# Kernel optimization log

Hardware: AMD Instinct MI355X
Metric: run time of the kernel (lower is better)

Reference implementation:

```python
import jax, jax.numpy as jnp
import numpy as np

B, T, C = 4, 2048, 1024
H, D = 16, 64  # num_heads, head_size; H*D == C


def setup_inputs() -> dict:
    key = jax.random.key(0)
    k1, k2, k3 = jax.random.split(key, 3)
    x = jax.random.normal(k1, (B, T, C), dtype=jnp.float32)
    w_qkv = jax.random.normal(k2, (C, 3 * C), dtype=jnp.float32) * (C ** -0.5)
    w_out = jax.random.normal(k3, (C, C), dtype=jnp.float32) * (C ** -0.5)
    b_out = jnp.zeros((C,), dtype=jnp.float32)
    return {"x": x, "w_qkv": w_qkv, "w_out": w_out, "b_out": b_out}


def reference(x, w_qkv, w_out, b_out):
    Bb, Tt, Cc = x.shape
    qkv = x @ w_qkv                        # [B,T,3C]
    q, k, v = jnp.split(qkv, 3, axis=2)
    # [B,T,C] -> [B,H,T,D]
    q = q.reshape(Bb, Tt, H, D).transpose(0, 2, 1, 3)
    k = k.reshape(Bb, Tt, H, D).transpose(0, 2, 1, 3)
    v = v.reshape(Bb, Tt, H, D).transpose(0, 2, 1, 3)
    scores = jnp.einsum('bhqd,bhkd->bhqk', q, k) * (D ** -0.5)
    causal = jnp.tril(jnp.ones((Tt, Tt), dtype=bool))
    scores = jnp.where(causal, scores, -jnp.inf)
    attn = jax.nn.softmax(scores, axis=-1)  # dropout is identity in eval mode
    out = jnp.einsum('bhqk,bhkd->bhqd', attn, v)
    out = out.transpose(0, 2, 1, 3).reshape(Bb, Tt, Cc)
    return out @ w_out + b_out
```

## Files before the change

kernel.cpp:

```cpp
#include <hip/hip_runtime.h>

typedef __bf16 bf16;
typedef __bf16 bf16x4 __attribute__((ext_vector_type(4)));
typedef __bf16 bf16x8 __attribute__((ext_vector_type(8)));
typedef float  f32x4  __attribute__((ext_vector_type(4)));

#define MFMA16(A_, B_, C_) __builtin_amdgcn_mfma_f32_16x16x32_bf16((A_), (B_), (C_), 0, 0, 0)

#define BB 4
#define TT 2048
#define CC 1024
#define HH 16
#define DD 64
#define MM (BB * TT)
#define N_QKV (3 * CC)
#define LDSS 72
#define BSTRIDE 36
#define QSCALE2 0.18033688f

#define BARRIER() do { asm volatile("" ::: "memory"); \
                       __builtin_amdgcn_s_barrier();  \
                       asm volatile("" ::: "memory"); } while (0)
#define VMCNT(n)  asm volatile("s_waitcnt vmcnt(" #n ")" ::: "memory")

static __device__ __forceinline__ void store_lds8(bf16* p, bf16x8 v) {
  bf16x4 lo, hi;
#pragma unroll
  for (int i = 0; i < 4; i++) { lo[i] = v[i]; hi[i] = v[i + 4]; }
  *(bf16x4*)p = lo;
  *(bf16x4*)(p + 4) = hi;
}

static __device__ __forceinline__ bf16x8 load_lds8(const bf16* p) {
  bf16x4 lo = *(const bf16x4*)p;
  bf16x4 hi = *(const bf16x4*)(p + 4);
  bf16x8 v;
#pragma unroll
  for (int i = 0; i < 4; i++) { v[i] = lo[i]; v[i + 4] = hi[i]; }
  return v;
}

static __device__ __forceinline__ void async_cp16(const bf16* g, bf16* l) {
  __builtin_amdgcn_global_load_lds(
      (const __attribute__((address_space(1))) void*)g,
      (__attribute__((address_space(3))) void*)l, 16, 0, 0);
}

__global__ __launch_bounds__(256) void sniff_k(const unsigned short* __restrict__ u,
                                               int* __restrict__ flag) {
  __shared__ int s;
  if (threadIdx.x == 0) s = 0;
  __syncthreads();
  int c = 0;
  for (int i = threadIdx.x; i < 65536; i += 256)
    if ((u[i] & 0x7F80u) == 0x7F80u) c = 1;
  if (c) atomicOr(&s, 1);
  __syncthreads();
  if (threadIdx.x == 0) *flag = s;
}

__global__ __launch_bounds__(256) void cvt_k(const void* __restrict__ in,
                                             bf16* __restrict__ out,
                                             const int* __restrict__ flag,
                                             size_t off) {
  const int fl = *flag;
  const size_t i = ((size_t)blockIdx.x * 256 + threadIdx.x) * 8;
  if (fl) {
    f32x4 a = *(const f32x4*)((const float*)in + off + i);
    f32x4 b = *(const f32x4*)((const float*)in + off + i + 4);
    bf16x8 o;
#pragma unroll
    for (int j = 0; j < 4; j++) { o[j] = (bf16)a[j]; o[4 + j] = (bf16)b[j]; }
    *(bf16x8*)(out + i) = o;
  } else {
    *(bf16x8*)(out + i) = *(const bf16x8*)((const bf16*)in + off + i);
  }
}

__global__ __launch_bounds__(256) void transpose_k(const void* __restrict__ in,
                                                   bf16* __restrict__ out,
                                                   int R, int C,
                                                   const int* __restrict__ flag) {
  __shared__ bf16 tile[32][33];
  const int fl = *flag;
  const int c0 = blockIdx.x * 32, r0 = blockIdx.y * 32;
  const int tx = threadIdx.x & 31, ty = threadIdx.x >> 5;
#pragma unroll
  for (int i = ty; i < 32; i += 8) {
    const size_t idx = (size_t)(r0 + i) * C + c0 + tx;
    tile[i][tx] = fl ? (bf16)((const float*)in)[idx] : ((const bf16*)in)[idx];
  }
  __syncthreads();
#pragma unroll
  for (int i = ty; i < 32; i += 8)
    out[(size_t)(c0 + i) * R + r0 + tx] = tile[tx][i];
}

__global__ __launch_bounds__(256) void vtrans_k(const bf16* __restrict__ qkv,
                                                bf16* __restrict__ vt) {
  __shared__ bf16 tile[32][33];
  const int bh = blockIdx.z;
  const int t0 = blockIdx.x * 32, d0 = blockIdx.y * 32;
  const bf16* src = qkv + (size_t)(bh >> 4) * TT * N_QKV + 2 * CC + (bh & 15) * DD;
  const int tx = threadIdx.x & 31, ty = threadIdx.x >> 5;
#pragma unroll
  for (int i = ty; i < 32; i += 8)
    tile[i][tx] = src[(size_t)(t0 + i) * N_QKV + d0 + tx];
  __syncthreads();
  bf16* dst = vt + ((size_t)bh * DD + d0) * TT + t0;
#pragma unroll
  for (int i = ty; i < 32; i += 8)
    dst[(size_t)i * TT + tx] = tile[tx][i];
}

template <int EPI>
__global__ __launch_bounds__(512, 2) void gemm8p2(const bf16* __restrict__ A,
                                                  const bf16* __restrict__ Bt,
                                                  const void* __restrict__ biasv,
                                                  void* __restrict__ Cv,
                                                  const int* __restrict__ flag,
                                                  int M, int N, int K,
                                                  int lda, int ldc) {
  __shared__ __align__(16) bf16 sAb[2][2][256 * 32];
  __shared__ __align__(16) bf16 sBb[2][2][128 * 32];
  const int fl = *flag;
  const int tid = threadIdx.x;
  const int lane = tid & 63, wave = tid >> 6;
  const int quad = lane >> 4, l15 = lane & 15;
  const int wm = wave >> 1, wn = wave & 1;

  const int nn = N >> 7;
  const int cpx = gridDim.x >> 3;
  const int sw = ((int)blockIdx.x & 7) * cpx + ((int)blockIdx.x >> 3);
  const int m0 = (sw / nn) * 256, n0 = (sw % nn) * 128;

  const int srow = tid >> 2;
  const int scol8 = (((tid & 3) ^ ((tid >> 3) & 3)) << 3);
  const int rdcol = ((quad ^ ((l15 >> 1) & 3)) << 3);

  const bf16* Asrc = A + (size_t)(m0 + srow) * lda + scol8;
  const bf16* Bsrc = Bt + (size_t)(n0 + srow) * K + scol8;

  f32x4 acc[4][4];
#pragma unroll
  for (int i = 0; i < 4; i++)
#pragma unroll
    for (int j = 0; j < 4; j++) {
      f32x4 z = {0.f, 0.f, 0.f, 0.f};
      acc[i][j] = z;
    }

#define ST_U(buf_, kk_, k0_) do {                                          \
    async_cp16(Asrc + (k0_) + (kk_) * 32, &sAb[buf_][kk_][wave * 512]);    \
    async_cp16(Asrc + (size_t)128 * lda + (k0_) + (kk_) * 32,              \
               &sAb[buf_][kk_][4096 + wave * 512]);                        \
    async_cp16(Bsrc + (k0_) + (kk_) * 32, &sBb[buf_][kk_][wave * 512]);    \
  } while (0)

#define PH2(buf_, kk_, STAGE_, WAIT_) do {                                   \
    bf16x8 af_[4], bf_[4];                                                   \
    _Pragma("unroll")                                                        \
    for (int mf = 0; mf < 4; mf++)                                           \
      af_[mf] = *(const bf16x8*)(&sAb[buf_][kk_][                            \
          (wm * 64 + mf * 16 + l15) * 32 + rdcol]);                          \
    _Pragma("unroll")                                                        \
    for (int nf = 0; nf < 4; nf++)                                           \
      bf_[nf] = *(const bf16x8*)(&sBb[buf_][kk_][                            \
          (wn * 64 + nf * 16 + l15) * 32 + rdcol]);                          \
    STAGE_;                                                                  \
    BARRIER();                                                               \
    __builtin_amdgcn_s_setprio(1);                                           \
    _Pragma("unroll")                                                        \
    for (int mf = 0; mf < 4; mf++)                                           \
      _Pragma("unroll")                                                      \
      for (int nf = 0; nf < 4; nf++)                                         \
        acc[mf][nf] = MFMA16(af_[mf], bf_[nf], acc[mf][nf]);                 \
    __builtin_amdgcn_s_setprio(0);                                           \
    WAIT_;                                                                   \
    BARRIER();                                                               \
  } while (0)

  ST_U(0, 0, 0);
  ST_U(0, 1, 0);
  ST_U(1, 0, 64);
  VMCNT(3);
  BARRIER();

  int k0 = 0;
  const int NI = (K >> 7) - 1;
  for (int i = 0; i < NI; i++, k0 += 128) {
    PH2(0, 0, ST_U(1, 1, k0 + 64),  VMCNT(6));
    PH2(0, 1, ST_U(0, 0, k0 + 128), VMCNT(6));
    PH2(1, 0, ST_U(0, 1, k0 + 128), VMCNT(6));
    PH2(1, 1, ST_U(1, 0, k0 + 192), VMCNT(6));
  }
  PH2(0, 0, ST_U(1, 1, k0 + 64), VMCNT(3));
  PH2(0, 1, ;,                   VMCNT(0));
  PH2(1, 0, ;,                   ;);
  PH2(1, 1, ;,                   ;);

#undef PH2
#undef ST_U

#pragma unroll
  for (int mf = 0; mf < 4; mf++) {
#pragma unroll
    for (int r = 0; r < 4; r++) {
      const int m = m0 + wm * 64 + mf * 16 + quad * 4 + r;
#pragma unroll
      for (int nf = 0; nf < 4; nf++) {
        const int n = n0 + wn * 64 + nf * 16 + l15;
        float v = acc[mf][nf][r];
        const size_t idx = (size_t)m * ldc + n;
        if (EPI == 1) {
          v += fl ? ((const float*)biasv)[n] : (float)((const bf16*)biasv)[n];
          if (fl) ((float*)Cv)[idx] = v;
          else    ((bf16*)Cv)[idx] = (bf16)v;
        } else {
          ((bf16*)Cv)[idx] = (bf16)v;
        }
      }
    }
  }
}

template <int EPI>
__global__ __launch_bounds__(256) void gemm_lds(const bf16* __restrict__ A,
                                                const bf16* __restrict__ Bt,
                                                const void* __restrict__ biasv,
                                                void* __restrict__ Cv,
                                                const int* __restrict__ flag,
                                                size_t aoff, size_t coff,
                                                int M, int N, int K,
                                                int lda, int ldc) {
  const int fl = *flag;
  __shared__ __align__(16) bf16 sA[128 * 32];
  __shared__ __align__(16) bf16 sB[128 * 32];
  const int tid = threadIdx.x;
  const int lane = tid & 63, wave = tid >> 6;
  const int quad = lane >> 4, l15 = lane & 15;
  const int wr = wave >> 1, wc = wave & 1;
  const int m0 = blockIdx.x * 128, n0 = blockIdx.y * 128;
  const int grow = lane >> 2;
  const int gcol = (lane & 3) * 8;

  f32x4 acc[4][4];
#pragma unroll
  for (int i = 0; i < 4; i++)
#pragma unroll
    for (int j = 0; j < 4; j++) {
      f32x4 z = {0.f, 0.f, 0.f, 0.f};
      acc[i][j] = z;
    }

  const bf16* Ag = A + aoff + (size_t)(m0 + wave * 32 + grow) * lda + gcol;
  const bf16* Bg = Bt + (size_t)(n0 + wave * 32 + grow) * K + gcol;
  bf16* sAw = sA + wave * 32 * 32;
  bf16* sBw = sB + wave * 32 * 32;

  for (int k0 = 0; k0 < K; k0 += 32) {
    __syncthreads();
    async_cp16(Ag, sAw);
    async_cp16(Ag + (size_t)16 * lda, sAw + 16 * 32);
    async_cp16(Bg, sBw);
    async_cp16(Bg + (size_t)16 * K, sBw + 16 * 32);
    Ag += 32;
    Bg += 32;
    __syncthreads();

    bf16x8 af[4], bfr[4];
#pragma unroll
    for (int mi = 0; mi < 4; mi++)
      af[mi] = *(const bf16x8*)(sA + (wr * 64 + mi * 16 + l15) * 32 + quad * 8);
#pragma unroll
    for (int ni = 0; ni < 4; ni++)
      bfr[ni] = *(const bf16x8*)(sB + (wc * 64 + ni * 16 + l15) * 32 + quad * 8);
#pragma unroll
    for (int mi = 0; mi < 4; mi++)
#pragma unroll
      for (int ni = 0; ni < 4; ni++)
        acc[mi][ni] = MFMA16(af[mi], bfr[ni], acc[mi][ni]);
  }

#pragma unroll
  for (int mi = 0; mi < 4; mi++) {
#pragma unroll
    for (int r = 0; r < 4; r++) {
      const int m = m0 + wr * 64 + mi * 16 + quad * 4 + r;
#pragma unroll
      for (int ni = 0; ni < 4; ni++) {
        const int n = n0 + wc * 64 + ni * 16 + l15;
        float v = acc[mi][ni][r];
        const size_t idx = coff + (size_t)m * ldc + n;
        if (EPI == 1) {
          v += fl ? ((const float*)biasv)[n] : (float)((const bf16*)biasv)[n];
          if (fl) ((float*)Cv)[idx] = v;
          else    ((bf16*)Cv)[idx] = (bf16)v;
        } else {
          ((bf16*)Cv)[idx] = (bf16)v;
        }
      }
    }
  }
}

template <int EPI, bool AF>
__global__ __launch_bounds__(256) void gemm_bt(const void* __restrict__ Av,
                                               const bf16* __restrict__ Bt,
                                               const void* __restrict__ biasv,
                                               void* __restrict__ Cv,
                                               const int* __restrict__ flag,
                                               size_t aoff, size_t coff,
                                               int M, int N, int K,
                                               int lda, int ldc) {
  const int fl = *flag;
  const bool af32 = AF && (fl != 0);
  __shared__ __align__(16) bf16 sA[128 * 32];
  __shared__ __align__(16) bf16 sB[128 * 32];
  const int tid = threadIdx.x;
  const int lane = tid & 63, wave = tid >> 6;
  const int quad = lane >> 4, l15 = lane & 15;
  const int wr = wave >> 1, wc = wave & 1;
  const int m0 = blockIdx.x * 128, n0 = blockIdx.y * 128;
  const int srow = tid >> 2;
  const int scol = (tid & 3) * 8;

  f32x4 acc[4][4];
#pragma unroll
  for (int i = 0; i < 4; i++)
#pragma unroll
    for (int j = 0; j < 4; j++) {
      f32x4 z = {0.f, 0.f, 0.f, 0.f};
      acc[i][j] = z;
    }

  const size_t abase0 = aoff + (size_t)(m0 + srow) * lda + scol;
  const size_t abase1 = abase0 + (size_t)64 * lda;
  const bf16* Bg0 = Bt + (size_t)(n0 + srow) * K + scol;
  const bf16* Bg1 = Bg0 + (size_t)64 * K;

  for (int k0 = 0; k0 < K; k0 += 32) {
    bf16x8 a0, a1;
    if (af32) {
      const float* Af = (const float*)Av;
      f32x4 p00 = *(const f32x4*)(Af + abase0 + k0);
      f32x4 p01 = *(const f32x4*)(Af + abase0 + k0 + 4);
      f32x4 p10 = *(const f32x4*)(Af + abase1 + k0);
      f32x4 p11 = *(const f32x4*)(Af + abase1 + k0 + 4);
#pragma unroll
      for (int i = 0; i < 4; i++) {
        a0[i] = (bf16)p00[i]; a0[i + 4] = (bf16)p01[i];
        a1[i] = (bf16)p10[i]; a1[i + 4] = (bf16)p11[i];
      }
    } else {
      const bf16* Ab = (const bf16*)Av;
      a0 = *(const bf16x8*)(Ab + abase0 + k0);
      a1 = *(const bf16x8*)(Ab + abase1 + k0);
    }
    bf16x8 b0 = *(const bf16x8*)(Bg0 + k0);
    bf16x8 b1 = *(const bf16x8*)(Bg1 + k0);
    __syncthreads();
    *(bf16x8*)(sA + srow * 32 + scol) = a0;
    *(bf16x8*)(sA + (64 + srow) * 32 + scol) = a1;
    *(bf16x8*)(sB + srow * 32 + scol) = b0;
    *(bf16x8*)(sB + (64 + srow) * 32 + scol) = b1;
    __syncthreads();

    bf16x8 af[4], bfr[4];
#pragma unroll
    for (int mi = 0; mi < 4; mi++)
      af[mi] = *(const bf16x8*)(sA + (wr * 64 + mi * 16 + l15) * 32 + quad * 8);
#pragma unroll
    for (int ni = 0; ni < 4; ni++)
      bfr[ni] = *(const bf16x8*)(sB + (wc * 64 + ni * 16 + l15) * 32 + quad * 8);
#pragma unroll
    for (int mi = 0; mi < 4; mi++)
#pragma unroll
      for (int ni = 0; ni < 4; ni++)
        acc[mi][ni] = MFMA16(af[mi], bfr[ni], acc[mi][ni]);
  }

#pragma unroll
  for (int mi = 0; mi < 4; mi++) {
#pragma unroll
    for (int r = 0; r < 4; r++) {
      const int m = m0 + wr * 64 + mi * 16 + quad * 4 + r;
#pragma unroll
      for (int ni = 0; ni < 4; ni++) {
        const int n = n0 + wc * 64 + ni * 16 + l15;
        float v = acc[mi][ni][r];
        const size_t idx = coff + (size_t)m * ldc + n;
        if (EPI == 1) {
          v += fl ? ((const float*)biasv)[n] : (float)((const bf16*)biasv)[n];
          if (fl) ((float*)Cv)[idx] = v;
          else    ((bf16*)Cv)[idx] = (bf16)v;
        } else {
          ((bf16*)Cv)[idx] = (bf16)v;
        }
      }
    }
  }
}

template <int EPI, bool AF, bool WF>
__global__ __launch_bounds__(256) void gemm_nt(const void* __restrict__ Av,
                                               const void* __restrict__ Wv,
                                               const void* __restrict__ biasv,
                                               void* __restrict__ Cv,
                                               const int* __restrict__ flag,
                                               size_t aoff, size_t coff,
                                               int M, int N, int K,
                                               int lda, int ldc) {
  const int fl = *flag;
  const bool af32 = AF && (fl != 0);
  const bool wf32 = WF && (fl != 0);
  __shared__ __align__(16) bf16 sA[128 * 32];
  __shared__ __align__(16) bf16 sB[128 * BSTRIDE];
  const int tid = threadIdx.x;
  const int lane = tid & 63, wave = tid >> 6;
  const int quad = lane >> 4, l15 = lane & 15;
  const int wr = wave >> 1, wc = wave & 1;
  const int m0 = blockIdx.x * 128, n0 = blockIdx.y * 128;
  const int arow = tid >> 2, acol = (tid & 3) * 8;
  const int wk = tid >> 3, wn = (tid & 7) * 16;

  f32x4 acc[4][4];
#pragma unroll
  for (int i = 0; i < 4; i++)
#pragma unroll
    for (int j = 0; j < 4; j++) {
      f32x4 z = {0.f, 0.f, 0.f, 0.f};
      acc[i][j] = z;
    }

  const size_t abase0 = aoff + (size_t)(m0 + arow) * lda + acol;
  const size_t abase1 = abase0 + (size_t)64 * lda;

  for (int k0 = 0; k0 < K; k0 += 32) {
    bf16x8 a0, a1;
    if (af32) {
      const float* Af = (const float*)Av;
      f32x4 p00 = *(const f32x4*)(Af + abase0 + k0);
      f32x4 p01 = *(const f32x4*)(Af + abase0 + k0 + 4);
      f32x4 p10 = *(const f32x4*)(Af + abase1 + k0);
      f32x4 p11 = *(const f32x4*)(Af + abase1 + k0 + 4);
#pragma unroll
      for (int i = 0; i < 4; i++) {
        a0[i] = (bf16)p00[i]; a0[i + 4] = (bf16)p01[i];
        a1[i] = (bf16)p10[i]; a1[i + 4] = (bf16)p11[i];
      }
    } else {
      const bf16* Ab = (const bf16*)Av;
      a0 = *(const bf16x8*)(Ab + abase0 + k0);
      a1 = *(const bf16x8*)(Ab + abase1 + k0);
    }
    bf16 wreg[16];
    const size_t wbase = (size_t)(k0 + wk) * N + n0 + wn;
    if (wf32) {
      const float* Wf = (const float*)Wv;
      f32x4 q0 = *(const f32x4*)(Wf + wbase);
      f32x4 q1 = *(const f32x4*)(Wf + wbase + 4);
      f32x4 q2 = *(const f32x4*)(Wf + wbase + 8);
      f32x4 q3 = *(const f32x4*)(Wf + wbase + 12);
#pragma unroll
      for (int i = 0; i < 4; i++) {
        wreg[i] = (bf16)q0[i];      wreg[4 + i] = (bf16)q1[i];
        wreg[8 + i] = (bf16)q2[i];  wreg[12 + i] = (bf16)q3[i];
      }
    } else {
      const bf16* Wb = (const bf16*)Wv;
      bf16x8 w0 = *(const bf16x8*)(Wb + wbase);
      bf16x8 w1 = *(const bf16x8*)(Wb + wbase + 8);
#pragma unroll
      for (int i = 0; i < 8; i++) { wreg[i] = w0[i]; wreg[8 + i] = w1[i]; }
    }
    __syncthreads();
    *(bf16x8*)(sA + arow * 32 + acol) = a0;
    *(bf16x8*)(sA + (64 + arow) * 32 + acol) = a1;
#pragma unroll
    for (int i = 0; i < 16; i++)
      sB[(wn + i) * BSTRIDE + wk] = wreg[i];
    __syncthreads();

    bf16x8 af[4], bfr[4];
#pragma unroll
    for (int mi = 0; mi < 4; mi++)
      af[mi] = *(const bf16x8*)(sA + (wr * 64 + mi * 16 + l15) * 32 + quad * 8);
#pragma unroll
    for (int ni = 0; ni < 4; ni++)
      bfr[ni] = load_lds8(sB + (wc * 64 + ni * 16 + l15) * BSTRIDE + quad * 8);
#pragma unroll
    for (int mi = 0; mi < 4; mi++)
#pragma unroll
      for (int ni = 0; ni < 4; ni++)
        acc[mi][ni] = MFMA16(af[mi], bfr[ni], acc[mi][ni]);
  }

#pragma unroll
  for (int mi = 0; mi < 4; mi++) {
#pragma unroll
    for (int r = 0; r < 4; r++) {
      const int m = m0 + wr * 64 + mi * 16 + quad * 4 + r;
#pragma unroll
      for (int ni = 0; ni < 4; ni++) {
        const int n = n0 + wc * 64 + ni * 16 + l15;
        float v = acc[mi][ni][r];
        const size_t idx = coff + (size_t)m * ldc + n;
        if (EPI == 1) {
          v += fl ? ((const float*)biasv)[n] : (float)((const bf16*)biasv)[n];
          if (fl) ((float*)Cv)[idx] = v;
          else    ((bf16*)Cv)[idx] = (bf16)v;
        } else {
          ((bf16*)Cv)[idx] = (bf16)v;
        }
      }
    }
  }
}

__global__ __launch_bounds__(256) void attn_k(bf16* __restrict__ qkv,
                                              const bf16* __restrict__ vt) {
  __shared__ __align__(16) bf16 sP[128 * LDSS];
  __shared__ __align__(16) bf16 sK[64 * LDSS];
  __shared__ __align__(16) bf16 sVt[64 * LDSS];

  const int tid = threadIdx.x;
  const int lane = tid & 63, wave = tid >> 6;
  const int quad = lane >> 4, l15 = lane & 15;
  const int bh = blockIdx.x;
  bf16* base = qkv + (size_t)(bh >> 4) * TT * N_QKV + (bh & 15) * DD;
  const bf16* Qp = base;
  const bf16* Kp = base + CC;
  const bf16* vhead = vt + (size_t)bh * DD * TT;

  const int qt = 15 - (int)blockIdx.y;
  const int q0 = qt * 128;
  const int wave_row0 = q0 + wave * 32;
  bf16* sPw = sP + (size_t)(wave * 32) * LDSS;

  const int krow = tid >> 2;
  const int kcol = (tid & 3) * 16;

  bf16x8 ones;
  {
    const bf16 o = (l15 == 0) ? (bf16)1.0f : (bf16)0.0f;
#pragma unroll
    for (int i = 0; i < 8; i++) ones[i] = o;
  }

  bf16x8 aq[2][2];
#pragma unroll
  for (int mi = 0; mi < 2; mi++)
#pragma unroll
    for (int ks = 0; ks < 2; ks++) {
      bf16x8 v = *(const bf16x8*)(Qp + (size_t)(wave_row0 + mi * 16 + l15) * N_QKV +
                                  ks * 32 + quad * 8);
#pragma unroll
      for (int i = 0; i < 8; i++) v[i] = (bf16)((float)v[i] * QSCALE2);
      aq[mi][ks] = v;
    }

  bf16x8 kr0, kr1, vr0, vr1;
  {
    const bf16* kp = Kp + (size_t)krow * N_QKV + kcol;
    kr0 = *(const bf16x8*)kp;
    kr1 = *(const bf16x8*)(kp + 8);
    const bf16* vp = vhead + (size_t)krow * TT + kcol;
    vr0 = *(const bf16x8*)vp;
    vr1 = *(const bf16x8*)(vp + 8);
  }

  f32x4 Oacc[2][4];
  f32x4 lacc[2];
#pragma unroll
  for (int mi = 0; mi < 2; mi++) {
    f32x4 z = {0.f, 0.f, 0.f, 0.f};
    lacc[mi] = z;
#pragma unroll
    for (int nt = 0; nt < 4; nt++) Oacc[mi][nt] = z;
  }

  const int jmax = q0 + 64;

  for (int j0 = 0; j0 <= jmax; j0 += 64) {
    __syncthreads();
    *(bf16x8*)(sK + krow * LDSS + kcol) = kr0;
    *(bf16x8*)(sK + krow * LDSS + kcol + 8) = kr1;
    *(bf16x8*)(sVt + krow * LDSS + kcol) = vr0;
    *(bf16x8*)(sVt + krow * LDSS + kcol + 8) = vr1;
    __syncthreads();

    if (j0 + 64 <= jmax) {
      const bf16* kp = Kp + (size_t)(j0 + 64 + krow) * N_QKV + kcol;
      kr0 = *(const bf16x8*)kp;
      kr1 = *(const bf16x8*)(kp + 8);
      const bf16* vp = vhead + (size_t)krow * TT + j0 + 64 + kcol;
      vr0 = *(const bf16x8*)vp;
      vr1 = *(const bf16x8*)(vp + 8);
    }

    if (j0 <= wave_row0 + 31) {
      f32x4 S[2][4];
#pragma unroll
      for (int mi = 0; mi < 2; mi++)
#pragma unroll
        for (int kt = 0; kt < 4; kt++) {
          f32x4 z = {0.f, 0.f, 0.f, 0.f};
          S[mi][kt] = z;
        }
      __builtin_amdgcn_s_setprio(1);
#pragma unroll
      for (int kt = 0; kt < 4; kt++) {
        const bf16* kp = sK + (size_t)(kt * 16 + l15) * LDSS + quad * 8;
        bf16x8 k0 = *(const bf16x8*)kp;
        bf16x8 k1 = *(const bf16x8*)(kp + 32);
        S[0][kt] = MFMA16(k0, aq[0][0], S[0][kt]);
        S[0][kt] = MFMA16(k1, aq[0][1], S[0][kt]);
        S[1][kt] = MFMA16(k0, aq[1][0], S[1][kt]);
        S[1][kt] = MFMA16(k1, aq[1][1], S[1][kt]);
      }
      __builtin_amdgcn_s_setprio(0);

      const bool needmask = (j0 + 63 > wave_row0);
#pragma unroll
      for (int mi = 0; mi < 2; mi++) {
        const int qg = wave_row0 + mi * 16 + l15;
#pragma unroll
        for (int kt = 0; kt < 4; kt++) {
          const int kb = j0 + kt * 16 + quad * 4;
          bf16x4 pk;
#pragma unroll
          for (int r = 0; r < 4; r++) {
            float e = __builtin_amdgcn_exp2f(S[mi][kt][r]);
            if (needmask && (kb + r > qg)) e = 0.f;
            pk[r] = (bf16)e;
          }
          *(bf16x4*)(sPw + (size_t)(mi * 16 + l15) * LDSS + kt * 16 + quad * 4) = pk;
        }
      }

      bf16x8 ap0[2], ap1[2];
#pragma unroll
      for (int mi = 0; mi < 2; mi++) {
        const bf16* pp = sPw + (size_t)(mi * 16 + l15) * LDSS + quad * 8;
        ap0[mi] = *(const bf16x8*)pp;
        ap1[mi] = *(const bf16x8*)(pp + 32);
      }
      __builtin_amdgcn_s_setprio(1);
#pragma unroll
      for (int mi = 0; mi < 2; mi++) {
        lacc[mi] = MFMA16(ap0[mi], ones, lacc[mi]);
        lacc[mi] = MFMA16(ap1[mi], ones, lacc[mi]);
      }
#pragma unroll
      for (int nt = 0; nt < 4; nt++) {
        const bf16* vp = sVt + (size_t)(nt * 16 + l15) * LDSS + quad * 8;
        bf16x8 v0 = *(const bf16x8*)vp;
        bf16x8 v1 = *(const bf16x8*)(vp + 32);
        Oacc[0][nt] = MFMA16(ap0[0], v0, Oacc[0][nt]);
        Oacc[0][nt] = MFMA16(ap1[0], v1, Oacc[0][nt]);
        Oacc[1][nt] = MFMA16(ap0[1], v0, Oacc[1][nt]);
        Oacc[1][nt] = MFMA16(ap1[1], v1, Oacc[1][nt]);
      }
      __builtin_amdgcn_s_setprio(0);
    }
  }

#pragma unroll
  for (int mi = 0; mi < 2; mi++)
#pragma unroll
    for (int r = 0; r < 4; r++) {
      const float lv = __shfl(lacc[mi][r], lane & 48, 64);
      const float invl = 1.0f / lv;
      const int t = q0 + wave * 32 + mi * 16 + quad * 4 + r;
#pragma unroll
      for (int nt = 0; nt < 4; nt++)
        base[(size_t)t * N_QKV + nt * 16 + l15] =
            (bf16)(Oacc[mi][nt][r] * invl);
    }
}

__global__ __launch_bounds__(256) void attn_s(bf16* __restrict__ qkv) {
  __shared__ __align__(16) bf16 sQ[128 * LDSS];
  __shared__ __align__(16) bf16 sK[64 * LDSS];
  __shared__ __align__(16) bf16 sVt[64 * LDSS];

  const int tid = threadIdx.x;
  const int lane = tid & 63, wave = tid >> 6;
  const int quad = lane >> 4, l15 = lane & 15;
  const int bh = blockIdx.x;
  bf16* base = qkv + (size_t)(bh >> 4) * TT * N_QKV + (bh & 15) * DD;
  const bf16* Qp = base;
  const bf16* Kp = base + CC;
  const bf16* Vp = base + 2 * CC;

  const int krow = tid >> 2;
  const int kcol = (tid & 3) * 16;
  const int vkey = tid & 31;
  const int vcol = (tid >> 5) * 8;

  bf16x8 ones;
  {
    const bf16 o = (l15 == 0) ? (bf16)1.0f : (bf16)0.0f;
#pragma unroll
    for (int i = 0; i < 8; i++) ones[i] = o;
  }

  const int qt = 15 - (int)blockIdx.y;
  const int q0 = qt * 128;

#pragma unroll
  for (int p = 0; p < 2; p++) {
    const int r = p * 64 + krow;
    const bf16* src = Qp + (size_t)(q0 + r) * N_QKV + kcol;
    bf16x8 v0 = *(const bf16x8*)src;
    bf16x8 v1 = *(const bf16x8*)(src + 8);
#pragma unroll
    for (int i = 0; i < 8; i++) {
      v0[i] = (bf16)((float)v0[i] * QSCALE2);
      v1[i] = (bf16)((float)v1[i] * QSCALE2);
    }
    *(bf16x8*)(sQ + r * LDSS + kcol) = v0;
    *(bf16x8*)(sQ + r * LDSS + kcol + 8) = v1;
  }

  bf16x8 kr0, kr1, vr0, vr1;
  {
    const bf16* kp = Kp + (size_t)krow * N_QKV + kcol;
    kr0 = *(const bf16x8*)kp;
    kr1 = *(const bf16x8*)(kp + 8);
    vr0 = *(const bf16x8*)(Vp + (size_t)vkey * N_QKV + vcol);
    vr1 = *(const bf16x8*)(Vp + (size_t)(32 + vkey) * N_QKV + vcol);
  }
  __syncthreads();

  bf16x8 aq[2][2];
#pragma unroll
  for (int mi = 0; mi < 2; mi++) {
    const bf16* qp = sQ + (size_t)(wave * 32 + mi * 16 + l15) * LDSS + quad * 8;
    aq[mi][0] = *(const bf16x8*)qp;
    aq[mi][1] = *(const bf16x8*)(qp + 32);
  }

  f32x4 Oacc[2][4];
  f32x4 lacc[2];
#pragma unroll
  for (int mi = 0; mi < 2; mi++) {
    f32x4 z = {0.f, 0.f, 0.f, 0.f};
    lacc[mi] = z;
#pragma unroll
    for (int nt = 0; nt < 4; nt++) Oacc[mi][nt] = z;
  }

  const int jmax = q0 + 64;
  const int wave_row0 = q0 + wave * 32;
  bf16* sP = sQ + (size_t)(wave * 32) * LDSS;

  for (int j0 = 0; j0 <= jmax; j0 += 64) {
    __syncthreads();
    *(bf16x8*)(sK + krow * LDSS + kcol) = kr0;
    *(bf16x8*)(sK + krow * LDSS + kcol + 8) = kr1;
#pragma unroll
    for (int i = 0; i < 8; i++) {
      sVt[(vcol + i) * LDSS + vkey] = vr0[i];
      sVt[(vcol + i) * LDSS + 32 + vkey] = vr1[i];
    }
    __syncthreads();

    if (j0 + 64 <= jmax) {
      const bf16* kp = Kp + (size_t)(j0 + 64 + krow) * N_QKV + kcol;
      kr0 = *(const bf16x8*)kp;
      kr1 = *(const bf16x8*)(kp + 8);
      vr0 = *(const bf16x8*)(Vp + (size_t)(j0 + 64 + vkey) * N_QKV + vcol);
      vr1 = *(const bf16x8*)(Vp + (size_t)(j0 + 96 + vkey) * N_QKV + vcol);
    }

    if (j0 <= wave_row0 + 31) {
      f32x4 S[2][4];
#pragma unroll
      for (int nt = 0; nt < 4; nt++) {
        const bf16* kp = sK + (size_t)(nt * 16 + l15) * LDSS + quad * 8;
        bf16x8 bk0 = *(const bf16x8*)kp;
        bf16x8 bk1 = *(const bf16x8*)(kp + 32);
#pragma unroll
        for (int mi = 0; mi < 2; mi++) {
          f32x4 acc = {0.f, 0.f, 0.f, 0.f};
          acc = MFMA16(aq[mi][0], bk0, acc);
          acc = MFMA16(aq[mi][1], bk1, acc);
          S[mi][nt] = acc;
        }
      }

      const bool needmask = (j0 + 63 > wave_row0);
#pragma unroll
      for (int mi = 0; mi < 2; mi++)
#pragma unroll
        for (int nt = 0; nt < 4; nt++) {
          const int kc = j0 + nt * 16 + l15;
#pragma unroll
          for (int r = 0; r < 4; r++) {
            float e = __builtin_amdgcn_exp2f(S[mi][nt][r]);
            if (needmask && kc > wave_row0 + mi * 16 + quad * 4 + r) e = 0.f;
            sP[(size_t)(mi * 16 + quad * 4 + r) * LDSS + nt * 16 + l15] =
                (bf16)e;
          }
        }

      bf16x8 ap[2][2];
#pragma unroll
      for (int mi = 0; mi < 2; mi++) {
        const bf16* pp = sP + (size_t)(mi * 16 + l15) * LDSS + quad * 8;
        ap[mi][0] = *(const bf16x8*)pp;
        ap[mi][1] = *(const bf16x8*)(pp + 32);
        lacc[mi] = MFMA16(ap[mi][0], ones, lacc[mi]);
        lacc[mi] = MFMA16(ap[mi][1], ones, lacc[mi]);
      }
#pragma unroll
      for (int nt = 0; nt < 4; nt++) {
        const bf16* vp = sVt + (size_t)(nt * 16 + l15) * LDSS + quad * 8;
        bf16x8 bv0 = *(const bf16x8*)vp;
        bf16x8 bv1 = *(const bf16x8*)(vp + 32);
#pragma unroll
        for (int mi = 0; mi < 2; mi++) {
          Oacc[mi][nt] = MFMA16(ap[mi][0], bv0, Oacc[mi][nt]);
          Oacc[mi][nt] = MFMA16(ap[mi][1], bv1, Oacc[mi][nt]);
        }
      }
    }
  }

#pragma unroll
  for (int mi = 0; mi < 2; mi++)
#pragma unroll
    for (int r = 0; r < 4; r++) {
      const float lv = __shfl(lacc[mi][r], lane & 48, 64);
      const float invl = 1.0f / lv;
      const int t = q0 + wave * 32 + mi * 16 + quad * 4 + r;
#pragma unroll
      for (int nt = 0; nt < 4; nt++)
        base[(size_t)t * N_QKV + nt * 16 + l15] =
            (bf16)(Oacc[mi][nt][r] * invl);
    }
}

extern "C" void kernel_launch(void* const* d_in, const int* in_sizes, int n_in,
                              void* d_out, int out_size, void* d_ws, size_t ws_size,
                              hipStream_t stream) {
  const void* x = d_in[0];
  const void* w_qkv = d_in[1];
  const void* w_out = d_in[2];
  const void* b_out = d_in[3];

  int* flag = (int*)d_ws;
  char* p = (char*)d_ws + 256;
  bf16* wqkvT = (bf16*)p;
  bf16* woutT = wqkvT + (size_t)N_QKV * CC;

  const size_t wT_bytes = ((size_t)N_QKV * CC + (size_t)CC * CC) * 2;
  const size_t qkv_bytes = (size_t)MM * N_QKV * 2;
  const size_t need_A = 256 + wT_bytes + qkv_bytes;
  const size_t need_B = 256 + wT_bytes + (size_t)TT * N_QKV * 2;

  sniff_k<<<1, 256, 0, stream>>>((const unsigned short*)x, flag);

  if (ws_size >= need_A) {
    bf16* qkv = woutT + (size_t)CC * CC;
    bf16* xb = qkv + (size_t)MM * N_QKV;
    const size_t slack = ws_size - need_A;

    transpose_k<<<dim3(N_QKV / 32, CC / 32), 256, 0, stream>>>(w_qkv, wqkvT, CC, N_QKV, flag);
    transpose_k<<<dim3(CC / 32, CC / 32), 256, 0, stream>>>(w_out, woutT, CC, CC, flag);

    const size_t full_xb = (size_t)MM * CC * 2;
    const size_t half_xb = full_xb / 2;
    if (slack >= full_xb) {
      cvt_k<<<(MM * CC) / 2048, 256, 0, stream>>>(x, xb, flag, 0);
      gemm8p2<0><<<dim3((MM / 256) * (N_QKV / 128)), 512, 0, stream>>>(
          xb, wqkvT, nullptr, qkv, flag, MM, N_QKV, CC, CC, N_QKV);
      bf16* vt = xb;
      vtrans_k<<<dim3(TT / 32, DD / 32, BB * HH), 256, 0, stream>>>(qkv, vt);
      attn_k<<<dim3(BB * HH, 16), 256, 0, stream>>>(qkv, vt);
    } else if (slack >= half_xb) {
      for (int m0 = 0; m0 < MM; m0 += 4096) {
        cvt_k<<<(4096 * CC) / 2048, 256, 0, stream>>>(x, xb, flag, (size_t)m0 * CC);
        gemm_lds<0><<<dim3(4096 / 128, N_QKV / 128), 256, 0, stream>>>(
            xb, wqkvT, nullptr, qkv, flag, 0, (size_t)m0 * N_QKV,
            4096, N_QKV, CC, CC, N_QKV);
      }
      attn_s<<<dim3(BB * HH, 16), 256, 0, stream>>>(qkv);
    } else {
      gemm_bt<0, true><<<dim3(MM / 128, N_QKV / 128), 256, 0, stream>>>(
          x, wqkvT, nullptr, qkv, flag, 0, 0, MM, N_QKV, CC, CC, N_QKV);
      attn_s<<<dim3(BB * HH, 16), 256, 0, stream>>>(qkv);
    }

    gemm8p2<1><<<dim3((MM / 256) * (CC / 128)), 512, 0, stream>>>(
        qkv, woutT, b_out, d_out, flag, MM, CC, CC, N_QKV, CC);
  } else if (ws_size >= need_B) {
    bf16* qkv = woutT + (size_t)CC * CC;
    transpose_k<<<dim3(N_QKV / 32, CC / 32), 256, 0, stream>>>(w_qkv, wqkvT, CC, N_QKV, flag);
    transpose_k<<<dim3(CC / 32, CC / 32), 256, 0, stream>>>(w_out, woutT, CC, CC, flag);
    for (int b = 0; b < BB; b++) {
      const size_t xoff = (size_t)b * TT * CC;
      gemm_bt<0, true><<<dim3(TT / 128, N_QKV / 128), 256, 0, stream>>>(
          x, wqkvT, nullptr, qkv, flag, xoff, 0, TT, N_QKV, CC, CC, N_QKV);
      attn_s<<<dim3(HH, 16), 256, 0, stream>>>(qkv);
      gemm_lds<1><<<dim3(TT / 128, CC / 128), 256, 0, stream>>>(
          qkv, woutT, b_out, d_out, flag, 0, xoff, TT, CC, CC, N_QKV, CC);
    }
  } else {
    bf16* qkvb = (bf16*)p;
    for (int b = 0; b < BB; b++) {
      const size_t xoff = (size_t)b * TT * CC;
      gemm_nt<0, true, true><<<dim3(TT / 128, N_QKV / 128), 256, 0, stream>>>(
          x, w_qkv, nullptr, qkvb, flag, xoff, 0, TT, N_QKV, CC, CC, N_QKV);
      attn_s<<<dim3(HH, 16), 256, 0, stream>>>(qkvb);
      gemm_nt<1, false, true><<<dim3(TT / 128, CC / 128), 256, 0, stream>>>(
          qkvb, w_out, b_out, d_out, flag, 0, xoff, TT, CC, CC, N_QKV, CC);
    }
  }
}
```

Baseline: 311.4 us.

## Add 256x256-tile 8-phase pipelined GEMM for the QKV projection

Adds a new gemm_q kernel that computes the QKV projection with 256x256 output tiles and a K-step of 64. Each block splits its tile into four 128x128 quadrants, loads them through double-buffered, XOR-swizzled LDS with async copies, and interleaves the loads with MFMA phases using barriers and s_setprio. Block indices are remapped in groups of eight to improve cache locality. The larger tile raises arithmetic intensity over the old 256x128 kernel, at the cost of more accumulator registers and LDS, which may limit occupancy.

```diff
diff --git a/kernel.cpp b/kernel.cpp
--- a/kernel.cpp
+++ b/kernel.cpp
@@ -111,6 +111,144 @@
 #pragma unroll
   for (int i = ty; i < 32; i += 8)
     dst[(size_t)i * TT + tx] = tile[tx][i];
+}
+
+__global__ __launch_bounds__(512, 2) void gemm_q(const bf16* __restrict__ A,
+                                                 const bf16* __restrict__ Bt,
+                                                 bf16* __restrict__ C,
+                                                 int M, int N, int K,
+                                                 int lda, int ldc) {
+  __shared__ __align__(16) bf16 sA[2][2][128 * 64];
+  __shared__ __align__(16) bf16 sB[2][2][128 * 64];
+  const int tid = threadIdx.x;
+  const int lane = tid & 63, wave = tid >> 6;
+  const int quad = lane >> 4, l15 = lane & 15;
+  const int wm = wave >> 2, wn = wave & 3;
+
+  const int nn = N >> 8;
+  const int cpx = gridDim.x >> 3;
+  const int sw = ((int)blockIdx.x & 7) * cpx + ((int)blockIdx.x >> 3);
+  const int m0 = (sw / nn) * 256, n0 = (sw % nn) * 256;
+
+  const int srow = tid >> 3;
+  const int scol = (((tid & 7) ^ ((tid >> 3) & 7)) << 3);
+  const int rdx = l15 & 7;
+
+  const bf16* Ag = A + (size_t)(m0 + srow) * lda + scol;
+  const bf16* Bg = Bt + (size_t)(n0 + srow) * K + scol;
+
+  f32x4 acc[2][2][4][2];
+#pragma unroll
+  for (int a = 0; a < 2; a++)
+#pragma unroll
+    for (int b = 0; b < 2; b++)
+#pragma unroll
+      for (int c = 0; c < 4; c++)
+#pragma unroll
+        for (int d = 0; d < 2; d++) {
+          f32x4 z = {0.f, 0.f, 0.f, 0.f};
+          acc[a][b][c][d] = z;
+        }
+
+  bf16x8 aq[2][4], bq0[2][2], bq1[2][2];
+
+#define STG_A(b_, h_, T_) do {                                               \
+    async_cp16(Ag + (size_t)((h_) * 128) * lda + (T_) * 64,                  \
+               &sA[b_][h_][wave * 512]);                                     \
+    async_cp16(Ag + (size_t)((h_) * 128 + 64) * lda + (T_) * 64,             \
+               &sA[b_][h_][4096 + wave * 512]);                              \
+  } while (0)
+#define STG_B(b_, h_, T_) do {                                               \
+    async_cp16(Bg + (size_t)((h_) * 128) * K + (T_) * 64,                    \
+               &sB[b_][h_][wave * 512]);                                     \
+    async_cp16(Bg + (size_t)((h_) * 128 + 64) * K + (T_) * 64,               \
+               &sB[b_][h_][4096 + wave * 512]);                              \
+  } while (0)
+#define RD_A(b_, h_) do {                                                    \
+    _Pragma("unroll")                                                        \
+    for (int kk = 0; kk < 2; kk++)                                           \
+      _Pragma("unroll")                                                      \
+      for (int mf = 0; mf < 4; mf++) {                                       \
+        const int r_ = wm * 64 + mf * 16 + l15;                              \
+        aq[kk][mf] = *(const bf16x8*)(&sA[b_][h_][                           \
+            r_ * 64 + (((kk * 4 + quad) ^ rdx) << 3)]);                      \
+      }                                                                      \
+  } while (0)
+#define RD_B(dst_, b_, h_) do {                                              \
+    _Pragma("unroll")                                                        \
+    for (int kk = 0; kk < 2; kk++)                                           \
+      _Pragma("unroll")                                                      \
+      for (int nf = 0; nf < 2; nf++) {                                       \
+        const int r_ = wn * 32 + nf * 16 + l15;                              \
+        dst_[kk][nf] = *(const bf16x8*)(&sB[b_][h_][                         \
+            r_ * 64 + (((kk * 4 + quad) ^ rdx) << 3)]);                      \
+      }                                                                      \
+  } while (0)
+#define PHASE(READS_, STAGE_, MH_, NH_, BQ_, WAIT_) do {                     \
+    READS_;                                                                  \
+    STAGE_;                                                                  \
+    BARRIER();                                                               \
+    __builtin_amdgcn_s_setprio(1);                                           \
+    _Pragma("unroll")                                                        \
+    for (int kk = 0; kk < 2; kk++)                                           \
+      _Pragma("unroll")                                                      \
+      for (int mf = 0; mf < 4; mf++)                                         \
+        _Pragma("unroll")                                                    \
+        for (int nf = 0; nf < 2; nf++)                                       \
+          acc[MH_][NH_][mf][nf] =                                            \
+              MFMA16(aq[kk][mf], BQ_[kk][nf], acc[MH_][NH_][mf][nf]);        \
+    __builtin_amdgcn_s_setprio(0);                                           \
+    WAIT_;                                                                   \
+    BARRIER();                                                               \
+  } while (0)
+
+  STG_A(0, 0, 0); STG_B(0, 0, 0); STG_B(0, 1, 0); STG_A(0, 1, 0);
+  STG_A(1, 0, 1); STG_B(1, 1, 1);
+  VMCNT(4);
+  BARRIER();
+
+  const int NIT = K >> 7;
+  int T = 0;
+  for (int i = 0; i < NIT - 1; i++, T += 2) {
+    PHASE({RD_A(0, 0); RD_B(bq0, 0, 0);}, STG_B(1, 0, T + 1), 0, 0, bq0, ;);
+    PHASE({RD_B(bq1, 0, 1);},             STG_A(1, 1, T + 1), 0, 1, bq1, ;);
+    PHASE({RD_A(0, 1);},                  STG_A(0, 0, T + 2), 1, 1, bq1, ;);
+    PHASE(;,                              STG_B(0, 1, T + 2), 1, 0, bq0, VMCNT(4));
+    PHASE({RD_A(1, 0); RD_B(bq0, 1, 0);}, STG_B(0, 0, T + 2), 0, 0, bq0, ;);
+    PHASE({RD_B(bq1, 1, 1);},             STG_A(0, 1, T + 2), 0, 1, bq1, ;);
+    PHASE({RD_A(1, 1);},                  STG_A(1, 0, T + 3), 1, 1, bq1, ;);
+    PHASE(;,                              STG_B(1, 1, T + 3), 1, 0, bq0, VMCNT(4));
+  }
+  PHASE({RD_A(0, 0); RD_B(bq0, 0, 0);}, STG_B(1, 0, T + 1), 0, 0, bq0, ;);
+  PHASE({RD_B(bq1, 0, 1);},             STG_A(1, 1, T + 1), 0, 1, bq1, ;);
+  PHASE({RD_A(0, 1);},                  ;,                   1, 1, bq1, ;);
+  PHASE(;,                              ;,                   1, 0, bq0, VMCNT(0));
+  PHASE({RD_A(1, 0); RD_B(bq0, 1, 0);}, ;,                   0, 0, bq0, ;);
+  PHASE({RD_B(bq1, 1, 1);},             ;,                   0, 1, bq1, ;);
+  PHASE({RD_A(1, 1);},                  ;,                   1, 1, bq1, ;);
+  PHASE(;,                              ;,                   1, 0, bq0, ;);
+
+#undef PHASE
+#undef RD_B
+#undef RD_A
+#undef STG_B
+#undef STG_A
+
+#pragma unroll
+  for (int MH = 0; MH < 2; MH++)
+#pragma unroll
+    for (int NH = 0; NH < 2; NH++)
+#pragma unroll
+      for (int mf = 0; mf < 4; mf++)
+#pragma unroll
+        for (int r = 0; r < 4; r++) {
+          const int m = m0 + MH * 128 + wm * 64 + mf * 16 + quad * 4 + r;
+#pragma unroll
+          for (int nf = 0; nf < 2; nf++) {
+            const int n = n0 + NH * 128 + wn * 32 + nf * 16 + l15;
+            C[(size_t)m * ldc + n] = (bf16)acc[MH][NH][mf][nf][r];
+          }
+        }
 }
 
 template <int EPI>
@@ -875,8 +1013,8 @@
     const size_t half_xb = full_xb / 2;
     if (slack >= full_xb) {
       cvt_k<<<(MM * CC) / 2048, 256, 0, stream>>>(x, xb, flag, 0);
-      gemm8p2<0><<<dim3((MM / 256) * (N_QKV / 128)), 512, 0, stream>>>(
-          xb, wqkvT, nullptr, qkv, flag, MM, N_QKV, CC, CC, N_QKV);
+      gemm_q<<<dim3((MM / 256) * (N_QKV / 256)), 512, 0, stream>>>(
+          xb, wqkvT, qkv, MM, N_QKV, CC, CC, N_QKV);
       bf16* vt = xb;
       vtrans_k<<<dim3(TT / 32, DD / 32, BB * HH), 256, 0, stream>>>(qkv, vt);
       attn_k<<<dim3(BB * HH, 16), 256, 0, stream>>>(qkv, vt);
```

Result: slower. 321.4 us (+3.2%).
